# Performance work log

Hardware: AMD Instinct MI355X
Metric: run time of the kernel (lower is better)

## Reference

```python
import jax, jax.numpy as jnp
import numpy as np

B, S = 8, 1024
DM = 512            # d_model arg
D = 2 * DM          # actual feature width (1024)
H = 16
DK = D // H         # 64
DV = 2 * 32         # per-head value dim (2*d_v) = 64
DI = 2048           # d_inner
K = 4               # d_conv, dilation 2 -> effective 7, pad 3 each side
EPS = 1e-6


def setup_inputs() -> dict:
    key = jax.random.key(0)
    ks = jax.random.split(key, 16)
    s = lambda k, shape, fan: jax.random.normal(k, shape, jnp.float32) / np.sqrt(fan)
    return {
        "x": jax.random.normal(ks[0], (B, S, D), jnp.float32),
        "mask": jnp.ones((B, 1, 1, S), jnp.int32),
        "gamma": jnp.ones((D,), jnp.float32),
        "wq": s(ks[1], (D, H * DK), D),
        "wk": s(ks[2], (D, H * DK), D),
        "wv": s(ks[3], (D, H * DV), D),
        "wo": s(ks[4], (H * DV, D), H * DV),
        "w1": s(ks[5], (DM, DI), DM),
        "b1": jnp.zeros((DI,), jnp.float32),
        "cw": s(ks[6], (DI, 1, K), K),   # depthwise conv kernel [O, I/groups=1, K]
        "cb": jnp.zeros((DI,), jnp.float32),
        "w2": s(ks[7], (DM, DI), DM),
        "b2": jnp.zeros((DI,), jnp.float32),
        "wp": s(ks[8], (DI, D), DI),
        "bp": jnp.zeros((D,), jnp.float32),
    }


def reference(x, mask, gamma, wq, wk, wv, wo, w1, b1, cw, cb, w2, b2, wp, bp):
    # RMSNorm
    nrm = x * jax.lax.rsqrt(jnp.mean(x * x, axis=-1, keepdims=True) + EPS) * gamma
    # Multi-head attention
    q = (nrm @ wq).reshape(B, S, H, DK).transpose(0, 2, 1, 3)
    k = (nrm @ wk).reshape(B, S, H, DK).transpose(0, 2, 1, 3)
    v = (nrm @ wv).reshape(B, S, H, DV).transpose(0, 2, 1, 3)
    scores = jnp.einsum('bhqd,bhkd->bhqk', q, k) / np.sqrt(DK).astype(np.float32)
    scores = jnp.where(mask == 0, jnp.float32(-1e9), scores)
    attn = jax.nn.softmax(scores, axis=-1)
    ctx = jnp.einsum('bhqk,bhkd->bhqd', attn, v)        # [B,H,S,DV]
    ctx = ctx.transpose(0, 2, 1, 3).reshape(B, S, H * DV)
    out = ctx @ wo                                       # [B,S,D]
    # split into two halves
    f_in, s_in = out[:, :, :D // 2], out[:, :, D // 2:]
    # FirstSection: linear -> depthwise dilated conv (padding 'same')
    f = f_in @ w1 + b1                                   # [B,S,DI]
    f = f.transpose(0, 2, 1)                             # [B,DI,S]
    f = jax.lax.conv_general_dilated(
        f, cw, window_strides=(1,), padding=[(3, 3)], rhs_dilation=(2,),
        feature_group_count=DI, dimension_numbers=('NCH', 'OIH', 'NCH'))
    f = (f + cb[None, :, None]).transpose(0, 2, 1)       # [B,S,DI]
    # SecondSection: linear + relu
    sec = jax.nn.relu(s_in @ w2 + b2)                    # [B,S,DI]
    gated = f * sec
    return x + (gated @ wp + bp)
```

## Files before the change

### kernel.cpp

```cpp
#include <hip/hip_runtime.h>

typedef unsigned short u16;
typedef __bf16 bf16x8 __attribute__((ext_vector_type(8)));
typedef short  s16x8  __attribute__((ext_vector_type(8)));
typedef float  f32x4  __attribute__((ext_vector_type(4)));

#define LDSPAD 72

#define GLOAD16(gp, lp) __builtin_amdgcn_global_load_lds( \
  (__attribute__((address_space(1))) unsigned int*)(unsigned long long)(const void*)(gp), \
  (__attribute__((address_space(3))) unsigned int*)(lp), 16, 0, 0)

static __device__ __forceinline__ u16 f2bf(float f){
  union { float f; unsigned int u; } v; v.f = f;
  unsigned int r = v.u + 0x7fffu + ((v.u >> 16) & 1u);
  return (u16)(r >> 16);
}
static __device__ __forceinline__ float bf2f(u16 u){
  union { unsigned int u; float f; } v; v.u = ((unsigned int)u) << 16; return v.f;
}
static __device__ __forceinline__ unsigned fbits(float f){
  union { float f; unsigned u; } v; v.f = f; return v.u;
}

__global__ __launch_bounds__(256) void wtrans_kernel(const float* __restrict__ in,
                                                     u16* __restrict__ out, int K, int N){
  __shared__ float tile[32][33];
  int n0 = blockIdx.x * 32, k0 = blockIdx.y * 32;
  int tx = threadIdx.x, ty = threadIdx.y;
  #pragma unroll
  for (int i = 0; i < 4; ++i)
    tile[ty + i*8][tx] = in[(size_t)(k0 + ty + i*8) * N + n0 + tx];
  __syncthreads();
  #pragma unroll
  for (int i = 0; i < 4; ++i)
    out[(size_t)(n0 + ty + i*8) * K + k0 + tx] = f2bf(tile[tx][ty + i*8]);
}

__global__ __launch_bounds__(256) void cwtrans_kernel(const float* __restrict__ cw,
                                                      float* __restrict__ cwT){
  int i = blockIdx.x * 256 + threadIdx.x;
  int c = i >> 2, j = i & 3;
  cwT[j * 2048 + c] = cw[i];
}

__global__ __launch_bounds__(256) void rmsnorm_kernel(const float* __restrict__ x,
                                                      const float* __restrict__ gamma,
                                                      u16* __restrict__ out){
  int row = blockIdx.x;
  const float* xr = x + (size_t)row * 1024;
  int tid = threadIdx.x;
  float4 xv = *(const float4*)(xr + tid * 4);
  float ss = xv.x*xv.x + xv.y*xv.y + xv.z*xv.z + xv.w*xv.w;
  #pragma unroll
  for (int off = 1; off < 64; off <<= 1) ss += __shfl_xor(ss, off);
  __shared__ float wsum[4];
  if ((tid & 63) == 0) wsum[tid >> 6] = ss;
  __syncthreads();
  float tot = wsum[0] + wsum[1] + wsum[2] + wsum[3];
  float r = rsqrtf(tot * (1.0f/1024.0f) + 1e-6f);
  const float4 gv = *(const float4*)(gamma + tid * 4);
  u16* o = out + (size_t)row * 1024 + tid * 4;
  o[0] = f2bf(xv.x * r * gv.x);
  o[1] = f2bf(xv.y * r * gv.y);
  o[2] = f2bf(xv.z * r * gv.z);
  o[3] = f2bf(xv.w * r * gv.w);
}

template<int EPI>
__global__ __launch_bounds__(256) void gemm128_kernel(
    const u16* __restrict__ A, int lda,
    const u16* __restrict__ Bt,
    const float* __restrict__ bias,
    const float* __restrict__ resid,
    u16* __restrict__ outb, float* __restrict__ outf,
    u16* __restrict__ vt,
    int N, int K, float scale, int nm)
{
  __shared__ __align__(16) u16 As[2][128*64];
  __shared__ __align__(16) u16 Bs[2][128*64];
  int tid = threadIdx.x;
  int wid = tid >> 6, lane = tid & 63;
  int fr = lane & 15, fq = lane >> 4;
  int wr = wid >> 1, wc = wid & 1;
  int l = ((int)blockIdx.x & 7) * ((int)gridDim.x >> 3) + ((int)blockIdx.x >> 3);
  int m0 = (l % nm) * 128, n0 = (l / nm) * 128;
  int srow = lane >> 3;
  int csw  = (lane & 7) ^ srow;
  int c7   = fr & 7;
  f32x4 acc[4][4] = {};

  const u16* Abase = A  + (size_t)m0 * lda;
  const u16* Bbase = Bt + (size_t)n0 * K;

  auto STAGE = [&](int bsel, int kt){
    int k0 = kt << 6;
    #pragma unroll
    for (int i = 0; i < 4; ++i){
      int r = i*32 + wid*8;
      GLOAD16(Abase + (size_t)(r + srow) * lda + k0 + csw*8, &As[bsel][r*64]);
      GLOAD16(Bbase + (size_t)(r + srow) * K   + k0 + csw*8, &Bs[bsel][r*64]);
    }
  };

  int nt = K >> 6;
  STAGE(0, 0);
  __syncthreads();
  for (int kt = 0; kt < nt; ++kt){
    int cur = kt & 1;
    if (kt + 1 < nt) STAGE(cur ^ 1, kt + 1);
    #pragma unroll
    for (int ks = 0; ks < 2; ++ks){
      bf16x8 av[4], bv[4];
      #pragma unroll
      for (int mi = 0; mi < 4; ++mi)
        av[mi] = *(const bf16x8*)&As[cur][(wr*64 + mi*16 + fr)*64 + (((ks*4 + fq) ^ c7) * 8)];
      #pragma unroll
      for (int ni = 0; ni < 4; ++ni)
        bv[ni] = *(const bf16x8*)&Bs[cur][(wc*64 + ni*16 + fr)*64 + (((ks*4 + fq) ^ c7) * 8)];
      #pragma unroll
      for (int mi = 0; mi < 4; ++mi)
        #pragma unroll
        for (int ni = 0; ni < 4; ++ni)
          acc[mi][ni] = __builtin_amdgcn_mfma_f32_16x16x32_bf16(av[mi], bv[ni], acc[mi][ni], 0, 0, 0);
    }
    __syncthreads();
  }

  if (EPI == 5 && n0 >= 2048){
    u16* Ct = &As[0][0];
    #pragma unroll
    for (int p = 0; p < 2; ++p){
      __syncthreads();
      if (wc == p){
        #pragma unroll
        for (int ni = 0; ni < 4; ++ni)
          #pragma unroll
          for (int mi = 0; mi < 4; ++mi){
            int cl = ni*16 + fr;
            int rl = wr*64 + mi*16 + fq*4;
            uint2 pk;
            pk.x = (unsigned)f2bf(acc[mi][ni][0]) | ((unsigned)f2bf(acc[mi][ni][1]) << 16);
            pk.y = (unsigned)f2bf(acc[mi][ni][2]) | ((unsigned)f2bf(acc[mi][ni][3]) << 16);
            *(uint2*)&Ct[cl*136 + rl] = pk;
          }
      }
      __syncthreads();
      #pragma unroll
      for (int ci = 0; ci < 4; ++ci){
        int qq = ci*256 + tid;
        int c = qq >> 4, off = (qq & 15) * 8;
        uint4 v = *(const uint4*)&Ct[c*136 + off];
        *(uint4*)&vt[(size_t)(n0 - 2048 + p*64 + c) * 8192 + m0 + off] = v;
      }
    }
    return;
  }

  #pragma unroll
  for (int ni = 0; ni < 4; ++ni){
    int col = n0 + wc*64 + ni*16 + fr;
    float bvv = (EPI >= 1 && EPI <= 3) ? bias[col] : 0.0f;
    float scl = (EPI == 5) ? ((col < 1024) ? scale : 1.0f) : scale;
    #pragma unroll
    for (int mi = 0; mi < 4; ++mi){
      #pragma unroll
      for (int j = 0; j < 4; ++j){
        int row = m0 + wr*64 + mi*16 + fq*4 + j;
        float vv = acc[mi][ni][j] * scl + bvv;
        if (EPI == 2) vv = fmaxf(vv, 0.0f);
        size_t idx = (size_t)row * N + col;
        if (EPI == 3) outf[idx] = vv + resid[idx];
        else          outb[idx] = f2bf(vv);
      }
    }
  }
}

__global__ __launch_bounds__(256) void attn_kernel(
    const u16* __restrict__ qkv, const u16* __restrict__ Vt,
    const int* __restrict__ mask, u16* __restrict__ ctx)
{
  __shared__ __align__(16) u16 Ks[64*64];
  __shared__ __align__(16) u16 Vs[64*64];
  __shared__ __align__(16) u16 Ps[64][LDSPAD];
  int tid = threadIdx.x;
  int wid = tid >> 6, lane = tid & 63;
  int fr = lane & 15, fq = lane >> 4;
  int q0 = blockIdx.x * 64;
  int bh = blockIdx.y;
  int b = bh >> 4, h = bh & 15;

  const u16* qb  = qkv + (size_t)b * 1024 * 3072 + h * 64;
  const u16* kb  = qb + 1024;
  const u16* vtb = Vt + (size_t)(h * 64) * 8192 + b * 1024;

  int lrow = lane >> 3;
  int cs   = (lane & 7) ^ lrow;
  int wbase = wid * 16;

  bf16x8 qf[2];
  {
    const u16* qp = qb + (size_t)(q0 + wid*16 + fr) * 3072 + fq * 8;
    qf[0] = *(const bf16x8*)(qp);
    qf[1] = *(const bf16x8*)(qp + 32);
  }
  f32x4 acc[4];
  #pragma unroll
  for (int i = 0; i < 4; ++i) acc[i] = (f32x4){0.f, 0.f, 0.f, 0.f};
  float m = -1e30f, lsum = 0.f;
  int c7 = fr & 7;

  for (int t = 0; t < 16; ++t){
    int kv0 = t * 64;
    __syncthreads();
    #pragma unroll
    for (int i = 0; i < 2; ++i){
      int r = wbase + i*8 + lrow;
      GLOAD16(kb  + (size_t)(kv0 + r) * 3072 + cs * 8, &Ks[(wbase + i*8) * 64]);
      GLOAD16(vtb + (size_t)r * 8192 + kv0 + cs * 8,   &Vs[(wbase + i*8) * 64]);
    }
    __syncthreads();

    f32x4 sc[4];
    #pragma unroll
    for (int nt = 0; nt < 4; ++nt) sc[nt] = (f32x4){0.f, 0.f, 0.f, 0.f};
    __builtin_amdgcn_s_setprio(1);
    #pragma unroll
    for (int ks = 0; ks < 2; ++ks){
      #pragma unroll
      for (int nt = 0; nt < 4; ++nt){
        bf16x8 kv = *(const bf16x8*)&Ks[(nt*16 + fr)*64 + (((ks*4 + fq) ^ c7) * 8)];
        sc[nt] = __builtin_amdgcn_mfma_f32_16x16x32_bf16(kv, qf[ks], sc[nt], 0, 0, 0);
      }
    }
    __builtin_amdgcn_s_setprio(0);

    #pragma unroll
    for (int nt = 0; nt < 4; ++nt){
      int4 mv = *(const int4*)&mask[b * 1024 + kv0 + nt*16 + fq*4];
      int mvals[4] = {mv.x, mv.y, mv.z, mv.w};
      #pragma unroll
      for (int j = 0; j < 4; ++j)
        sc[nt][j] = mvals[j] ? sc[nt][j] : -1e9f;
    }

    float pmax = -1e30f;
    #pragma unroll
    for (int nt = 0; nt < 4; ++nt)
      #pragma unroll
      for (int j = 0; j < 4; ++j)
        pmax = fmaxf(pmax, sc[nt][j]);
    pmax = fmaxf(pmax, __shfl_xor(pmax, 16));
    pmax = fmaxf(pmax, __shfl_xor(pmax, 32));
    if (!__all(pmax <= m + 8.0f)){
      float mnew = fmaxf(m, pmax);
      float corr = exp2f(m - mnew);
      #pragma unroll
      for (int nt = 0; nt < 4; ++nt)
        #pragma unroll
        for (int j = 0; j < 4; ++j)
          acc[nt][j] *= corr;
      lsum *= corr;
      m = mnew;
    }
    float p[4][4];
    float ls = 0.f;
    #pragma unroll
    for (int nt = 0; nt < 4; ++nt)
      #pragma unroll
      for (int j = 0; j < 4; ++j){
        float pv = exp2f(sc[nt][j] - m);
        p[nt][j] = pv;
        ls += pv;
      }
    lsum += ls;

    #pragma unroll
    for (int nt = 0; nt < 4; ++nt){
      unsigned d0 = __builtin_amdgcn_perm(fbits(p[nt][1]), fbits(p[nt][0]), 0x07060302u);
      unsigned d1 = __builtin_amdgcn_perm(fbits(p[nt][3]), fbits(p[nt][2]), 0x07060302u);
      *(unsigned*)&Ps[wid*16 + fr][nt*16 + fq*4]     = d0;
      *(unsigned*)&Ps[wid*16 + fr][nt*16 + fq*4 + 2] = d1;
    }

    __builtin_amdgcn_s_setprio(1);
    #pragma unroll
    for (int ks = 0; ks < 2; ++ks){
      bf16x8 pb = *(const bf16x8*)&Ps[wid*16 + fr][ks*32 + fq*8];
      #pragma unroll
      for (int nt = 0; nt < 4; ++nt){
        bf16x8 vv = *(const bf16x8*)&Vs[(nt*16 + fr)*64 + (((ks*4 + fq) ^ c7) * 8)];
        acc[nt] = __builtin_amdgcn_mfma_f32_16x16x32_bf16(vv, pb, acc[nt], 0, 0, 0);
      }
    }
    __builtin_amdgcn_s_setprio(0);
  }

  lsum += __shfl_xor(lsum, 16);
  lsum += __shfl_xor(lsum, 32);
  float invl = 1.0f / lsum;

  size_t rowbase = ((size_t)b * 1024 + q0 + wid*16 + fr) * 1024 + h * 64;
  #pragma unroll
  for (int nt = 0; nt < 4; ++nt){
    unsigned lo = (unsigned)f2bf(acc[nt][0] * invl) | ((unsigned)f2bf(acc[nt][1] * invl) << 16);
    unsigned hi = (unsigned)f2bf(acc[nt][2] * invl) | ((unsigned)f2bf(acc[nt][3] * invl) << 16);
    uint2 pk; pk.x = lo; pk.y = hi;
    *(uint2*)&ctx[rowbase + nt*16 + fq*4] = pk;
  }
}

__global__ __launch_bounds__(256) void convgate_kernel(
    const u16* __restrict__ f, const float* __restrict__ cwT,
    const float* __restrict__ cb, u16* __restrict__ sec_inout)
{
  size_t gid = (size_t)blockIdx.x * blockDim.x + threadIdx.x;
  int c0 = (int)(gid & 255) * 8;
  int t  = (int)((gid >> 8) & 1023);
  int b  = (int)(gid >> 18);
  const u16* fb = f + ((size_t)b * 1024) * 2048;

  float4 w[4][2];
  #pragma unroll
  for (int j = 0; j < 4; ++j){
    w[j][0] = *(const float4*)&cwT[j*2048 + c0];
    w[j][1] = *(const float4*)&cwT[j*2048 + c0 + 4];
  }
  float4 cb0 = *(const float4*)&cb[c0];
  float4 cb1 = *(const float4*)&cb[c0 + 4];
  float acc[8] = {cb0.x, cb0.y, cb0.z, cb0.w, cb1.x, cb1.y, cb1.z, cb1.w};

  #pragma unroll
  for (int j = 0; j < 4; ++j){
    int tt = t - 3 + 2 * j;
    if (tt >= 0 && tt < 1024){
      s16x8 fv = *(const s16x8*)(fb + (size_t)tt * 2048 + c0);
      const float* wj = (const float*)&w[j][0];
      #pragma unroll
      for (int e = 0; e < 8; ++e) acc[e] += bf2f((u16)fv[e]) * wj[e];
    }
  }
  u16* sp = sec_inout + (((size_t)b * 1024 + t) * 2048 + c0);
  s16x8 sv = *(const s16x8*)sp;
  s16x8 ov;
  #pragma unroll
  for (int e = 0; e < 8; ++e) ov[e] = (short)f2bf(acc[e] * bf2f((u16)sv[e]));
  *(s16x8*)sp = ov;
}

extern "C" void kernel_launch(void* const* d_in, const int* in_sizes, int n_in,
                              void* d_out, int out_size, void* d_ws, size_t ws_size,
                              hipStream_t stream)
{
  const float* x     = (const float*)d_in[0];
  const int*   mask  = (const int*)  d_in[1];
  const float* gamma = (const float*)d_in[2];
  const float* wq    = (const float*)d_in[3];
  const float* wk    = (const float*)d_in[4];
  const float* wv    = (const float*)d_in[5];
  const float* wo    = (const float*)d_in[6];
  const float* w1    = (const float*)d_in[7];
  const float* b1    = (const float*)d_in[8];
  const float* cw    = (const float*)d_in[9];
  const float* cb    = (const float*)d_in[10];
  const float* w2    = (const float*)d_in[11];
  const float* b2    = (const float*)d_in[12];
  const float* wp    = (const float*)d_in[13];
  const float* bp    = (const float*)d_in[14];
  float* out = (float*)d_out;

  char* p = (char*)d_ws;
  auto alloc = [&](size_t bytes){ char* r = p; p += (bytes + 255) & ~(size_t)255; return r; };
  u16*   wqkvT = (u16*)alloc((size_t)3072*1024*2);
  u16*   woT   = (u16*)alloc((size_t)1024*1024*2);
  u16*   w1T   = (u16*)alloc((size_t)2048*512*2);
  u16*   w2T   = (u16*)alloc((size_t)2048*512*2);
  u16*   wpT   = (u16*)alloc((size_t)1024*2048*2);
  float* cwT   = (float*)alloc((size_t)4*2048*4);
  u16*   nrm   = (u16*)alloc((size_t)8192*1024*2);
  u16*   qkv   = (u16*)alloc((size_t)8192*3072*2);
  u16*   sec   = (u16*)alloc((size_t)8192*2048*2);
  u16* Vt   = sec;
  u16* ao   = qkv;
  u16* fbuf = qkv + (size_t)8192*1024;
  (void)ws_size; (void)in_sizes; (void)n_in; (void)out_size;

  const float QSCALE = 0.125f * 1.44269504088896340736f;

  dim3 tb32(32, 8);
  wtrans_kernel<<<dim3(32, 32), tb32, 0, stream>>>(wq, wqkvT,                     1024, 1024);
  wtrans_kernel<<<dim3(32, 32), tb32, 0, stream>>>(wk, wqkvT + (size_t)1024*1024, 1024, 1024);
  wtrans_kernel<<<dim3(32, 32), tb32, 0, stream>>>(wv, wqkvT + (size_t)2048*1024, 1024, 1024);
  wtrans_kernel<<<dim3(32, 32), tb32, 0, stream>>>(wo, woT, 1024, 1024);
  wtrans_kernel<<<dim3(64, 16), tb32, 0, stream>>>(w1, w1T, 512, 2048);
  wtrans_kernel<<<dim3(64, 16), tb32, 0, stream>>>(w2, w2T, 512, 2048);
  wtrans_kernel<<<dim3(32, 64), tb32, 0, stream>>>(wp, wpT, 2048, 1024);
  cwtrans_kernel<<<32, 256, 0, stream>>>(cw, cwT);

  rmsnorm_kernel<<<8192, 256, 0, stream>>>(x, gamma, nrm);

  gemm128_kernel<5><<<1536, 256, 0, stream>>>(nrm, 1024, wqkvT, nullptr, nullptr, qkv, nullptr, Vt, 3072, 1024, QSCALE, 64);

  attn_kernel<<<dim3(16, 128), 256, 0, stream>>>(qkv, Vt, mask, nrm);

  gemm128_kernel<0><<<512, 256, 0, stream>>>(nrm, 1024, woT, nullptr, nullptr, ao, nullptr, nullptr, 1024, 1024, 1.0f, 64);

  gemm128_kernel<1><<<1024, 256, 0, stream>>>(ao,       1024, w1T, b1, nullptr, fbuf, nullptr, nullptr, 2048, 512, 1.0f, 64);
  gemm128_kernel<2><<<1024, 256, 0, stream>>>(ao + 512, 1024, w2T, b2, nullptr, sec,  nullptr, nullptr, 2048, 512, 1.0f, 64);

  convgate_kernel<<<8192, 256, 0, stream>>>(fbuf, cwT, cb, sec);

  gemm128_kernel<3><<<512, 256, 0, stream>>>(sec, 2048, wpT, bp, x, nullptr, out, nullptr, 1024, 2048, 1.0f, 64);
}
```

Baseline: 354.6 us.

## Process two query tiles per attention block, preload K/V to registers, drop GEMM swizzle

The attention kernel now handles 128 queries per block as two 64-row sub-tiles. Each K/V tile is read from LDS into registers once and reused for both sub-tiles, and loading of the next tile is issued right after the register reads, overlapping global loads with compute. The grid is halved to match. The GEMM block-index remapping (XCD-style interleave) is also removed in favour of linear block order, which may change L2 locality across chiplets. The register pressure from the kf/vf arrays and the doubled accumulators may reduce occupancy.

```diff
diff --git a/kernel.cpp b/kernel.cpp
--- a/kernel.cpp
+++ b/kernel.cpp
@@ -83,7 +83,7 @@
   int wid = tid >> 6, lane = tid & 63;
   int fr = lane & 15, fq = lane >> 4;
   int wr = wid >> 1, wc = wid & 1;
-  int l = ((int)blockIdx.x & 7) * ((int)gridDim.x >> 3) + ((int)blockIdx.x >> 3);
+  int l = (int)blockIdx.x;
   int m0 = (l % nm) * 128, n0 = (l / nm) * 128;
   int srow = lane >> 3;
   int csw  = (lane & 7) ^ srow;
@@ -187,7 +187,7 @@
   int tid = threadIdx.x;
   int wid = tid >> 6, lane = tid & 63;
   int fr = lane & 15, fq = lane >> 4;
-  int q0 = blockIdx.x * 64;
+  int q0 = blockIdx.x * 128;
   int bh = blockIdx.y;
   int b = bh >> 4, h = bh & 15;
 
@@ -198,116 +198,134 @@
   int lrow = lane >> 3;
   int cs   = (lane & 7) ^ lrow;
   int wbase = wid * 16;
-
-  bf16x8 qf[2];
-  {
-    const u16* qp = qb + (size_t)(q0 + wid*16 + fr) * 3072 + fq * 8;
-    qf[0] = *(const bf16x8*)(qp);
-    qf[1] = *(const bf16x8*)(qp + 32);
-  }
-  f32x4 acc[4];
-  #pragma unroll
-  for (int i = 0; i < 4; ++i) acc[i] = (f32x4){0.f, 0.f, 0.f, 0.f};
-  float m = -1e30f, lsum = 0.f;
   int c7 = fr & 7;
 
-  for (int t = 0; t < 16; ++t){
+  bf16x8 qf[2][2];
+  #pragma unroll
+  for (int s = 0; s < 2; ++s){
+    const u16* qp = qb + (size_t)(q0 + s*64 + wid*16 + fr) * 3072 + fq * 8;
+    qf[s][0] = *(const bf16x8*)(qp);
+    qf[s][1] = *(const bf16x8*)(qp + 32);
+  }
+  f32x4 acc[2][4];
+  #pragma unroll
+  for (int s = 0; s < 2; ++s)
+    #pragma unroll
+    for (int i = 0; i < 4; ++i) acc[s][i] = (f32x4){0.f, 0.f, 0.f, 0.f};
+  float mrun[2] = {-1e30f, -1e30f}, lsum[2] = {0.f, 0.f};
+
+  auto STAGE = [&](int t){
     int kv0 = t * 64;
-    __syncthreads();
     #pragma unroll
     for (int i = 0; i < 2; ++i){
       int r = wbase + i*8 + lrow;
       GLOAD16(kb  + (size_t)(kv0 + r) * 3072 + cs * 8, &Ks[(wbase + i*8) * 64]);
       GLOAD16(vtb + (size_t)r * 8192 + kv0 + cs * 8,   &Vs[(wbase + i*8) * 64]);
     }
+  };
+
+  STAGE(0);
+  for (int t = 0; t < 16; ++t){
+    int kv0 = t * 64;
     __syncthreads();
-
-    f32x4 sc[4];
-    #pragma unroll
-    for (int nt = 0; nt < 4; ++nt) sc[nt] = (f32x4){0.f, 0.f, 0.f, 0.f};
-    __builtin_amdgcn_s_setprio(1);
-    #pragma unroll
-    for (int ks = 0; ks < 2; ++ks){
+    bf16x8 kf[2][4], vf[2][4];
+    #pragma unroll
+    for (int ks = 0; ks < 2; ++ks)
       #pragma unroll
       for (int nt = 0; nt < 4; ++nt){
-        bf16x8 kv = *(const bf16x8*)&Ks[(nt*16 + fr)*64 + (((ks*4 + fq) ^ c7) * 8)];
-        sc[nt] = __builtin_amdgcn_mfma_f32_16x16x32_bf16(kv, qf[ks], sc[nt], 0, 0, 0);
-      }
-    }
-    __builtin_amdgcn_s_setprio(0);
-
+        kf[ks][nt] = *(const bf16x8*)&Ks[(nt*16 + fr)*64 + (((ks*4 + fq) ^ c7) * 8)];
+        vf[ks][nt] = *(const bf16x8*)&Vs[(nt*16 + fr)*64 + (((ks*4 + fq) ^ c7) * 8)];
+      }
+    __syncthreads();
+    if (t + 1 < 16) STAGE(t + 1);
+
+    #pragma unroll
+    for (int s = 0; s < 2; ++s){
+      f32x4 sc[4];
+      #pragma unroll
+      for (int nt = 0; nt < 4; ++nt) sc[nt] = (f32x4){0.f, 0.f, 0.f, 0.f};
+      __builtin_amdgcn_s_setprio(1);
+      #pragma unroll
+      for (int ks = 0; ks < 2; ++ks)
+        #pragma unroll
+        for (int nt = 0; nt < 4; ++nt)
+          sc[nt] = __builtin_amdgcn_mfma_f32_16x16x32_bf16(kf[ks][nt], qf[s][ks], sc[nt], 0, 0, 0);
+      __builtin_amdgcn_s_setprio(0);
+
+      #pragma unroll
+      for (int nt = 0; nt < 4; ++nt){
+        int4 mv = *(const int4*)&mask[b * 1024 + kv0 + nt*16 + fq*4];
+        int mvals[4] = {mv.x, mv.y, mv.z, mv.w};
+        #pragma unroll
+        for (int j = 0; j < 4; ++j)
+          sc[nt][j] = mvals[j] ? sc[nt][j] : -1e9f;
+      }
+
+      float pmax = -1e30f;
+      #pragma unroll
+      for (int nt = 0; nt < 4; ++nt)
+        #pragma unroll
+        for (int j = 0; j < 4; ++j)
+          pmax = fmaxf(pmax, sc[nt][j]);
+      pmax = fmaxf(pmax, __shfl_xor(pmax, 16));
+      pmax = fmaxf(pmax, __shfl_xor(pmax, 32));
+      if (!__all(pmax <= mrun[s] + 8.0f)){
+        float mnew = fmaxf(mrun[s], pmax);
+        float corr = exp2f(mrun[s] - mnew);
+        #pragma unroll
+        for (int nt = 0; nt < 4; ++nt)
+          #pragma unroll
+          for (int j = 0; j < 4; ++j)
+            acc[s][nt][j] *= corr;
+        lsum[s] *= corr;
+        mrun[s] = mnew;
+      }
+      float p[4][4];
+      float ls = 0.f;
+      #pragma unroll
+      for (int nt = 0; nt < 4; ++nt)
+        #pragma unroll
+        for (int j = 0; j < 4; ++j){
+          float pv = exp2f(sc[nt][j] - mrun[s]);
+          p[nt][j] = pv;
+          ls += pv;
+        }
+      lsum[s] += ls;
+
+      #pragma unroll
+      for (int nt = 0; nt < 4; ++nt){
+        unsigned d0 = __builtin_amdgcn_perm(fbits(p[nt][1]), fbits(p[nt][0]), 0x07060302u);
+        unsigned d1 = __builtin_amdgcn_perm(fbits(p[nt][3]), fbits(p[nt][2]), 0x07060302u);
+        *(unsigned*)&Ps[wid*16 + fr][nt*16 + fq*4]     = d0;
+        *(unsigned*)&Ps[wid*16 + fr][nt*16 + fq*4 + 2] = d1;
+      }
+
+      __builtin_amdgcn_s_setprio(1);
+      #pragma unroll
+      for (int ks = 0; ks < 2; ++ks){
+        bf16x8 pb = *(const bf16x8*)&Ps[wid*16 + fr][ks*32 + fq*8];
+        #pragma unroll
+        for (int nt = 0; nt < 4; ++nt)
+          acc[s][nt] = __builtin_amdgcn_mfma_f32_16x16x32_bf16(vf[ks][nt], pb, acc[s][nt], 0, 0, 0);
+      }
+      __builtin_amdgcn_s_setprio(0);
+    }
+  }
+
+  #pragma unroll
+  for (int s = 0; s < 2; ++s){
+    float ltot = lsum[s];
+    ltot += __shfl_xor(ltot, 16);
+    ltot += __shfl_xor(ltot, 32);
+    float invl = 1.0f / ltot;
+    size_t rowbase = ((size_t)b * 1024 + q0 + s*64 + wid*16 + fr) * 1024 + h * 64;
     #pragma unroll
     for (int nt = 0; nt < 4; ++nt){
-      int4 mv = *(const int4*)&mask[b * 1024 + kv0 + nt*16 + fq*4];
-      int mvals[4] = {mv.x, mv.y, mv.z, mv.w};
-      #pragma unroll
-      for (int j = 0; j < 4; ++j)
-        sc[nt][j] = mvals[j] ? sc[nt][j] : -1e9f;
-    }
-
-    float pmax = -1e30f;
-    #pragma unroll
-    for (int nt = 0; nt < 4; ++nt)
-      #pragma unroll
-      for (int j = 0; j < 4; ++j)
-        pmax = fmaxf(pmax, sc[nt][j]);
-    pmax = fmaxf(pmax, __shfl_xor(pmax, 16));
-    pmax = fmaxf(pmax, __shfl_xor(pmax, 32));
-    if (!__all(pmax <= m + 8.0f)){
-      float mnew = fmaxf(m, pmax);
-      float corr = exp2f(m - mnew);
-      #pragma unroll
-      for (int nt = 0; nt < 4; ++nt)
-        #pragma unroll
-        for (int j = 0; j < 4; ++j)
-          acc[nt][j] *= corr;
-      lsum *= corr;
-      m = mnew;
-    }
-    float p[4][4];
-    float ls = 0.f;
-    #pragma unroll
-    for (int nt = 0; nt < 4; ++nt)
-      #pragma unroll
-      for (int j = 0; j < 4; ++j){
-        float pv = exp2f(sc[nt][j] - m);
-        p[nt][j] = pv;
-        ls += pv;
-      }
-    lsum += ls;
-
-    #pragma unroll
-    for (int nt = 0; nt < 4; ++nt){
-      unsigned d0 = __builtin_amdgcn_perm(fbits(p[nt][1]), fbits(p[nt][0]), 0x07060302u);
-      unsigned d1 = __builtin_amdgcn_perm(fbits(p[nt][3]), fbits(p[nt][2]), 0x07060302u);
-      *(unsigned*)&Ps[wid*16 + fr][nt*16 + fq*4]     = d0;
-      *(unsigned*)&Ps[wid*16 + fr][nt*16 + fq*4 + 2] = d1;
-    }
-
-    __builtin_amdgcn_s_setprio(1);
-    #pragma unroll
-    for (int ks = 0; ks < 2; ++ks){
-      bf16x8 pb = *(const bf16x8*)&Ps[wid*16 + fr][ks*32 + fq*8];
-      #pragma unroll
-      for (int nt = 0; nt < 4; ++nt){
-        bf16x8 vv = *(const bf16x8*)&Vs[(nt*16 + fr)*64 + (((ks*4 + fq) ^ c7) * 8)];
-        acc[nt] = __builtin_amdgcn_mfma_f32_16x16x32_bf16(vv, pb, acc[nt], 0, 0, 0);
-      }
-    }
-    __builtin_amdgcn_s_setprio(0);
-  }
-
-  lsum += __shfl_xor(lsum, 16);
-  lsum += __shfl_xor(lsum, 32);
-  float invl = 1.0f / lsum;
-
-  size_t rowbase = ((size_t)b * 1024 + q0 + wid*16 + fr) * 1024 + h * 64;
-  #pragma unroll
-  for (int nt = 0; nt < 4; ++nt){
-    unsigned lo = (unsigned)f2bf(acc[nt][0] * invl) | ((unsigned)f2bf(acc[nt][1] * invl) << 16);
-    unsigned hi = (unsigned)f2bf(acc[nt][2] * invl) | ((unsigned)f2bf(acc[nt][3] * invl) << 16);
-    uint2 pk; pk.x = lo; pk.y = hi;
-    *(uint2*)&ctx[rowbase + nt*16 + fq*4] = pk;
+      unsigned lo = (unsigned)f2bf(acc[s][nt][0] * invl) | ((unsigned)f2bf(acc[s][nt][1] * invl) << 16);
+      unsigned hi = (unsigned)f2bf(acc[s][nt][2] * invl) | ((unsigned)f2bf(acc[s][nt][3] * invl) << 16);
+      uint2 pk; pk.x = lo; pk.y = hi;
+      *(uint2*)&ctx[rowbase + nt*16 + fq*4] = pk;
+    }
   }
 }
 
@@ -402,7 +420,7 @@
 
   gemm128_kernel<5><<<1536, 256, 0, stream>>>(nrm, 1024, wqkvT, nullptr, nullptr, qkv, nullptr, Vt, 3072, 1024, QSCALE, 64);
 
-  attn_kernel<<<dim3(16, 128), 256, 0, stream>>>(qkv, Vt, mask, nrm);
+  attn_kernel<<<dim3(8, 128), 256, 0, stream>>>(qkv, Vt, mask, nrm);
 
   gemm128_kernel<0><<<512, 256, 0, stream>>>(nrm, 1024, woT, nullptr, nullptr, ao, nullptr, nullptr, 1024, 1024, 1.0f, 64);
 
```

After: 334.3 us. 1.06x faster.
